# Optimization experiments

Hardware: AMD Instinct MI355X
Metric: run time of the kernel (lower is better)

Reference implementation:

```python
import jax, jax.numpy as jnp
import numpy as np

B, S, D = 8, 1024, 1024
H, Dh = 16, 64
NEG = 1e12


def setup_inputs() -> dict:
    key = jax.random.key(0)
    ks = jax.random.split(key, 8)
    scale = 0.02
    return {
        "Q": jax.random.normal(ks[0], (B, S, D), dtype=jnp.float32),
        "K": jax.random.normal(ks[1], (B, S, D), dtype=jnp.float32),
        "V": jax.random.normal(ks[2], (B, S, D), dtype=jnp.float32),
        "WQ": jax.random.normal(ks[3], (D, H * Dh), dtype=jnp.float32) * scale,
        "WK": jax.random.normal(ks[4], (D, H * Dh), dtype=jnp.float32) * scale,
        "WV": jax.random.normal(ks[5], (D, H * Dh), dtype=jnp.float32) * scale,
        "Q_len": jax.random.randint(ks[6], (B, 1), 0, S, dtype=jnp.int32),
        "V_len": jax.random.randint(ks[7], (B, 1), 0, S, dtype=jnp.int32),
    }


def reference(Q, K, V, WQ, WK, WV, Q_len, V_len):
    b, sq, _ = Q.shape
    sk = K.shape[1]
    # QKV projections -> [B, H, S, Dh]
    q = (Q @ WQ).reshape(b, sq, H, Dh).transpose(0, 2, 1, 3)
    k = (K @ WK).reshape(b, sk, H, Dh).transpose(0, 2, 1, 3)
    v = (V @ WV).reshape(b, sk, H, Dh).transpose(0, 2, 1, 3)
    # scaled scores [B, H, Sq, Sk]
    A = jnp.einsum("bhqd,bhkd->bhqk", q, k) / jnp.sqrt(jnp.float32(Dh))
    # key padding mask: valid where position < V_len (one_hot + cumsum equivalent)
    key_valid = (jnp.arange(sk)[None, :] < V_len[:, 0:1]).astype(A.dtype)  # [B, Sk]
    A = A - (1.0 - key_valid)[:, None, None, :] * NEG
    # causal mask (mask_right=True): mask strictly upper triangle
    causal = (jnp.arange(sq)[:, None] < jnp.arange(sk)[None, :]).astype(A.dtype)
    A = A - causal[None, None, :, :] * NEG
    A = jax.nn.softmax(A, axis=-1)
    O = jnp.einsum("bhqk,bhkd->bhqd", A, v)
    O = O.transpose(0, 2, 1, 3).reshape(b, sq, H * Dh)
    # query mask (multiplicative)
    q_valid = (jnp.arange(sq)[None, :] < Q_len[:, 0:1]).astype(O.dtype)  # [B, Sq]
    return O * q_valid[:, :, None]
```

## Files before the change

### kernel.cpp

```cpp
#include <hip/hip_runtime.h>
#include <hip/hip_bf16.h>


#define B_  8
#define S_  1024
#define D_  1024
#define H_  16
#define DH_ 64

using f16x8  = __attribute__((ext_vector_type(8))) _Float16;
using h16x2  = __attribute__((ext_vector_type(2))) __fp16;
using s16x8  = __attribute__((ext_vector_type(8))) short;
using f32x4  = __attribute__((ext_vector_type(4))) float;
using s16x4  = __attribute__((ext_vector_type(4))) short;

__device__ inline short f2h(float x) {
  _Float16 h = (_Float16)x;
  return __builtin_bit_cast(short, h);
}

__device__ inline unsigned pk2(float a, float b) {
  h16x2 p = __builtin_amdgcn_cvt_pkrtz(a, b);
  return __builtin_bit_cast(unsigned, p);
}

__device__ inline f16x8 ld_frag_g(const short* p) {
  return __builtin_bit_cast(f16x8, *(const s16x8*)p);
}

__device__ inline int kvlim_of(int vl, int ql) {
  const int v = (vl == 0) ? S_ : vl;
  return (v < ql) ? v : ql;
}

#define GLOAD_LDS16(gsrc, ldst)                                              \
  __builtin_amdgcn_global_load_lds(                                          \
      (const __attribute__((address_space(1))) unsigned int*)(gsrc),         \
      (__attribute__((address_space(3))) unsigned int*)(ldst), 16, 0, 0)

__global__ __launch_bounds__(256) void prep(
    const float* __restrict__ Qx, const float* __restrict__ Kx,
    const float* __restrict__ Vx, const float* __restrict__ WQ,
    const float* __restrict__ WK, const float* __restrict__ WV,
    short* __restrict__ dq, short* __restrict__ dk, short* __restrict__ dv,
    short* __restrict__ wt, short* __restrict__ qp, int* __restrict__ alist,
    const int* __restrict__ Qlen, const int* __restrict__ Vlen) {
  __shared__ float t[64][65];
  __shared__ int scnt[257];
  const int bid = blockIdx.x;
  const int tid = threadIdx.x;
  if (bid == 3840) {
    int ql[8], kv[8];
#pragma unroll
    for (int b = 0; b < 8; ++b) {
      ql[b] = Qlen[b];
      kv[b] = kvlim_of(Vlen[b], ql[b]);
    }
    int loc[6];
    int cnt = 0;
#pragma unroll
    for (int k = 0; k < 6; ++k) {
      const int c = tid * 6 + k;
      const int slice = c % 3, r = c / 3;
      bool act;
      if (slice < 2) {
        const int jm = r & 63;
        const int m0 = (jm & 7) * 1024 + (jm >> 3) * 128;
        const int len = slice ? kv[m0 >> 10] : ql[m0 >> 10];
        act = (m0 & 1023) < len;
      } else {
        const int jn = r >> 3;
        const int n0 = (jn & 7) * 1024 + (jn >> 3) * 128;
        act = (n0 & 1023) < kv[n0 >> 10];
      }
      if (act) loc[cnt++] = c;
    }
    scnt[tid] = cnt;
    __syncthreads();
    if (tid == 0) {
      int s = 0;
      for (int i = 0; i < 256; ++i) {
        const int v = scnt[i];
        scnt[i] = s;
        s += v;
      }
      scnt[256] = s;
    }
    __syncthreads();
    const int base = scnt[tid];
    for (int k = 0; k < cnt; ++k) alist[base + k] = loc[k];
    if (tid == 0) alist[1536] = scnt[256];
  } else if (bid < 3072) {
    const int slice = bid >> 10;
    const int tok0 = (bid & 1023) * 8;
    const int bb = tok0 >> 10, local = tok0 & 1023;
    const int ql = Qlen[bb];
    int lim;
    if (slice == 0) {
      lim = (ql + 127) & ~127;
    } else {
      lim = (kvlim_of(Vlen[bb], ql) + 127) & ~127;
    }
    if (local >= lim) {
      if (slice == 0) {
        const uint4 zz = {0u, 0u, 0u, 0u};
        const int hh = tid >> 4;
        short* zp = qp + ((size_t)((bb * H_ + hh) * S_) + local) * DH_ +
                    (tid & 15) * 32;
        *(uint4*)(zp + 0) = zz;
        *(uint4*)(zp + 8) = zz;
        *(uint4*)(zp + 16) = zz;
        *(uint4*)(zp + 24) = zz;
      }
      return;
    }
    const float* src = (slice == 0) ? Qx : (slice == 1) ? Kx : Vx;
    short* dst = (slice == 0) ? dq : (slice == 1) ? dk : dv;
    const size_t base = (size_t)(bid & 1023) * 8192;
#pragma unroll
    for (int j = 0; j < 4; ++j) {
      const size_t off = base + (size_t)j * 2048 + (size_t)tid * 8;
      float4 a = *(const float4*)(src + off);
      float4 b = *(const float4*)(src + off + 4);
      uint4 u = {pk2(a.x, a.y), pk2(a.z, a.w), pk2(b.x, b.y), pk2(b.z, b.w)};
      *(uint4*)(dst + off) = u;
    }
  } else {
    const int wid = bid - 3072;
    const int slice = wid >> 8;
    const int rem = wid & 255;
    const int n0 = (rem & 15) * 64, k0 = (rem >> 4) * 64;
    const float* W = (slice == 0) ? WQ : (slice == 1) ? WK : WV;
    {
      const int r = tid >> 2, c4 = tid & 3;
#pragma unroll
      for (int j = 0; j < 4; ++j) {
        float4 v = *(const float4*)(W + (size_t)(k0 + r) * D_ + n0 + c4 * 16 +
                                    j * 4);
        t[r][c4 * 16 + j * 4 + 0] = v.x;
        t[r][c4 * 16 + j * 4 + 1] = v.y;
        t[r][c4 * 16 + j * 4 + 2] = v.z;
        t[r][c4 * 16 + j * 4 + 3] = v.w;
      }
    }
    __syncthreads();
    {
      const int rn = tid >> 2, ks = tid & 3;
      short* dst =
          wt + ((size_t)slice << 20) + (size_t)(n0 + rn) * D_ + k0 + ks * 16;
      s16x4 h[4];
#pragma unroll
      for (int g = 0; g < 4; ++g)
#pragma unroll
        for (int j = 0; j < 4; ++j) h[g][j] = f2h(t[ks * 16 + g * 4 + j][rn]);
      *(s16x4*)(dst + 0) = h[0];
      *(s16x4*)(dst + 4) = h[1];
      *(s16x4*)(dst + 8) = h[2];
      *(s16x4*)(dst + 12) = h[3];
    }
  }
}

__global__ __launch_bounds__(256, 3) void proj(
    const short* __restrict__ xq, const short* __restrict__ xk,
    const short* __restrict__ xv, const short* __restrict__ wt,
    short* __restrict__ qp, short* __restrict__ kp, short* __restrict__ vp,
    const int* __restrict__ alist) {
  __shared__ __align__(16) short As[3][128][32];
  __shared__ __align__(16) short Bs[3][128][32];
  const int gid = blockIdx.x;
  if (gid >= alist[1536]) return;
  const int c = alist[gid];
  const int slice = c % 3;
  const int r = c / 3;
  const int tid = threadIdx.x;
  const short* A;
  const short* Bp;
  int m0, n0;
  float oscale;
  if (slice < 2) {
    A = slice ? xk : xq;
    Bp = wt + ((size_t)slice << 20);
    const int jm = r & 63;
    m0 = (jm & 7) * 1024 + (jm >> 3) * 128;
    n0 = (r >> 6) * 128;
    oscale = slice ? 1.0f : 0.125f;
  } else {
    A = wt + ((size_t)2 << 20);
    Bp = xv;
    m0 = (r & 7) * 128;
    const int jn = r >> 3;
    n0 = (jn & 7) * 1024 + (jn >> 3) * 128;
    oscale = 1.0f;
  }

  const int lane = tid & 63, w = tid >> 6;
  const int wr = w >> 1, wc = w & 1;
  const int lr = lane & 15, lg = lane >> 4;
  const int g_row = tid >> 2, g_c = tid & 3;
  const int gsw = (g_c ^ ((g_row >> 1) & 3)) * 8;
  const int rsw = (lg ^ ((lr >> 1) & 3)) * 8;

  const short* ga = A + (size_t)(m0 + g_row) * D_ + gsw;
  const short* gb = Bp + (size_t)(n0 + g_row) * D_ + gsw;

  f32x4 acc[4][4];
#pragma unroll
  for (int i = 0; i < 4; ++i)
#pragma unroll
    for (int j = 0; j < 4; ++j) acc[i][j] = f32x4{0.f, 0.f, 0.f, 0.f};

  GLOAD_LDS16(ga, &As[0][g_row][g_c * 8]);
  GLOAD_LDS16(ga + (size_t)64 * D_, &As[0][g_row + 64][g_c * 8]);
  GLOAD_LDS16(gb, &Bs[0][g_row][g_c * 8]);
  GLOAD_LDS16(gb + (size_t)64 * D_, &Bs[0][g_row + 64][g_c * 8]);
  GLOAD_LDS16(ga + 32, &As[1][g_row][g_c * 8]);
  GLOAD_LDS16(ga + (size_t)64 * D_ + 32, &As[1][g_row + 64][g_c * 8]);
  GLOAD_LDS16(gb + 32, &Bs[1][g_row][g_c * 8]);
  GLOAD_LDS16(gb + (size_t)64 * D_ + 32, &Bs[1][g_row + 64][g_c * 8]);

  for (int kt = 0; kt < 32; ++kt) {
    const int cur = kt % 3;
    if (kt < 30)
      asm volatile("s_waitcnt vmcnt(4)" ::: "memory");
    else
      asm volatile("s_waitcnt vmcnt(0)" ::: "memory");
    __builtin_amdgcn_s_barrier();
    __builtin_amdgcn_sched_barrier(0);
    if (kt < 30) {
      const int pre = (kt + 2) % 3;
      const int k2 = (kt + 2) * 32;
      GLOAD_LDS16(ga + k2, &As[pre][g_row][g_c * 8]);
      GLOAD_LDS16(ga + (size_t)64 * D_ + k2, &As[pre][g_row + 64][g_c * 8]);
      GLOAD_LDS16(gb + k2, &Bs[pre][g_row][g_c * 8]);
      GLOAD_LDS16(gb + (size_t)64 * D_ + k2, &Bs[pre][g_row + 64][g_c * 8]);
    }

    f16x8 af[4], bf[4];
#pragma unroll
    for (int mi = 0; mi < 4; ++mi)
      af[mi] = ld_frag_g(&As[cur][wr * 64 + mi * 16 + lr][rsw]);
#pragma unroll
    for (int ni = 0; ni < 4; ++ni)
      bf[ni] = ld_frag_g(&Bs[cur][wc * 64 + ni * 16 + lr][rsw]);
#pragma unroll
    for (int mi = 0; mi < 4; ++mi)
#pragma unroll
      for (int ni = 0; ni < 4; ++ni)
        acc[mi][ni] = __builtin_amdgcn_mfma_f32_16x16x32_f16(
            af[mi], bf[ni], acc[mi][ni], 0, 0, 0);
  }

  short* outp = (slice == 0) ? qp : kp;
#pragma unroll
  for (int mi = 0; mi < 4; ++mi)
#pragma unroll
    for (int ni = 0; ni < 4; ++ni) {
      const int mg0 = m0 + wr * 64 + mi * 16 + lg * 4;
      const int ng = n0 + wc * 64 + ni * 16 + lr;
#pragma unroll
      for (int reg = 0; reg < 4; ++reg) {
        const int m = mg0 + reg;
        const short val = f2h(acc[mi][ni][reg] * oscale);
        if (slice < 2) {
          const int b = m >> 10, s = m & 1023, hh = ng >> 6, dh = ng & 63;
          outp[((size_t)((b * H_ + hh) * S_) + s) * DH_ + dh] = val;
        } else {
          vp[((size_t)(ng >> 10) << 20) + (size_t)m * S_ + (ng & 1023)] = val;
        }
      }
    }
}

__global__ __launch_bounds__(256, 2) void attn_fwd(
    const short* __restrict__ qp, const short* __restrict__ kp,
    const short* __restrict__ vT, const int* __restrict__ Qlen,
    const int* __restrict__ Vlen, float* __restrict__ out) {
  __shared__ short Plds[2][4][16][72];
  const int bid = blockIdx.x;
  const int z = bid & 7;
  const int bh = bid >> 3;
  const int h = bh & 15;
  const int b = bh >> 4;
  const int lane = threadIdx.x & 63;
  const int w = threadIdx.x >> 6;
  const int lr = lane & 15, lg = lane >> 4;
  const short* qb = qp + (size_t)((b * H_ + h) * S_) * DH_;
  const short* kb = kp + (size_t)((b * H_ + h) * S_) * DH_;
  const short* vb = vT + (size_t)((b * H_ + h) * DH_) * S_;
  const int vlen = Vlen[b], qlen = Qlen[b];

  const int qtH = 15 - z, qtL = z;
  const int vcap = (vlen + 63) >> 6;
  const int nTH = (vlen > 0) ? min(qtH + 1, vcap) : (qtH + 1);
  const int nTL = (vlen > 0) ? min(qtL + 1, vcap) : (qtL + 1);
  const int q0H = qtH * 64 + w * 16;
  const int q0L = qtL * 64 + w * 16;

  const bool hAct = qlen > qtH * 64;
  const bool lAct = qlen > qtL * 64;
  const int tHn = hAct ? nTH : 0;
  const int tLn = lAct ? nTL : 0;
  const int tMax = (tHn > tLn) ? tHn : tLn;

  f16x8 qfH[2], qfL[2];
#pragma unroll
  for (int c = 0; c < 2; ++c) {
    qfH[c] = ld_frag_g(qb + (size_t)(q0H + lr) * DH_ + c * 32 + lg * 8);
    qfL[c] = ld_frag_g(qb + (size_t)(q0L + lr) * DH_ + c * 32 + lg * 8);
  }

  float lH[4], lL[4];
  f32x4 oH[4], oL[4];
#pragma unroll
  for (int rr = 0; rr < 4; ++rr) {
    lH[rr] = 0.f; lL[rr] = 0.f;
    oH[rr] = f32x4{0.f, 0.f, 0.f, 0.f};
    oL[rr] = f32x4{0.f, 0.f, 0.f, 0.f};
  }

  f16x8 kf[8];
#pragma unroll
  for (int nt = 0; nt < 4; ++nt)
#pragma unroll
    for (int c = 0; c < 2; ++c)
      kf[nt * 2 + c] =
          ld_frag_g(kb + (size_t)(nt * 16 + lr) * DH_ + c * 32 + lg * 8);

  for (int t = 0; t < tMax; ++t) {
    const int kv0 = t * 64;
    const int kvn = (t + 1 < tMax) ? kv0 + 64 : kv0;
    const bool hact = t < tHn;
    const bool lact = t < tLn;

    f16x8 vf[8];
#pragma unroll
    for (int dt = 0; dt < 4; ++dt)
#pragma unroll
      for (int c = 0; c < 2; ++c)
        vf[dt * 2 + c] =
            ld_frag_g(vb + (size_t)(dt * 16 + lr) * S_ + kv0 + c * 32 + lg * 8);

    f16x8 kn[8];
#pragma unroll
    for (int nt = 0; nt < 4; ++nt)
#pragma unroll
      for (int c = 0; c < 2; ++c)
        kn[nt * 2 + c] = ld_frag_g(kb + (size_t)(kvn + nt * 16 + lr) * DH_ +
                                   c * 32 + lg * 8);

    const bool km = (vlen > 0) && (vlen - kv0 < 64);

    f32x4 sH[4], sL[4];
    if (hact) {
#pragma unroll
      for (int nt = 0; nt < 4; ++nt) sH[nt] = f32x4{0.f, 0.f, 0.f, 0.f};
#pragma unroll
      for (int nt = 0; nt < 4; ++nt)
#pragma unroll
        for (int c = 0; c < 2; ++c)
          sH[nt] = __builtin_amdgcn_mfma_f32_16x16x32_f16(
              qfH[c], kf[nt * 2 + c], sH[nt], 0, 0, 0);
    }
    if (lact) {
#pragma unroll
      for (int nt = 0; nt < 4; ++nt) sL[nt] = f32x4{0.f, 0.f, 0.f, 0.f};
#pragma unroll
      for (int nt = 0; nt < 4; ++nt)
#pragma unroll
        for (int c = 0; c < 2; ++c)
          sL[nt] = __builtin_amdgcn_mfma_f32_16x16x32_f16(
              qfL[c], kf[nt * 2 + c], sL[nt], 0, 0, 0);
    }

    if (hact) {
      if ((t == qtH) | km) {
#pragma unroll
        for (int reg = 0; reg < 4; ++reg) {
          const int qrow = q0H + lg * 4 + reg;
#pragma unroll
          for (int nt = 0; nt < 4; ++nt) {
            const int kv = kv0 + nt * 16 + lr;
            float sv = sH[nt][reg];
            if (km && kv >= vlen) sv -= 1e12f;
            if (kv > qrow) sv -= 1e12f;
            const float p = __expf(sv);
            lH[reg] += p;
            Plds[0][w][lg * 4 + reg][nt * 16 + lr] = f2h(p);
          }
        }
      } else {
#pragma unroll
        for (int reg = 0; reg < 4; ++reg)
#pragma unroll
          for (int nt = 0; nt < 4; ++nt) {
            const float p = __expf(sH[nt][reg]);
            lH[reg] += p;
            Plds[0][w][lg * 4 + reg][nt * 16 + lr] = f2h(p);
          }
      }
    }
    if (lact) {
      if ((t == qtL) | km) {
#pragma unroll
        for (int reg = 0; reg < 4; ++reg) {
          const int qrow = q0L + lg * 4 + reg;
#pragma unroll
          for (int nt = 0; nt < 4; ++nt) {
            const int kv = kv0 + nt * 16 + lr;
            float sv = sL[nt][reg];
            if (km && kv >= vlen) sv -= 1e12f;
            if (kv > qrow) sv -= 1e12f;
            const float p = __expf(sv);
            lL[reg] += p;
            Plds[1][w][lg * 4 + reg][nt * 16 + lr] = f2h(p);
          }
        }
      } else {
#pragma unroll
        for (int reg = 0; reg < 4; ++reg)
#pragma unroll
          for (int nt = 0; nt < 4; ++nt) {
            const float p = __expf(sL[nt][reg]);
            lL[reg] += p;
            Plds[1][w][lg * 4 + reg][nt * 16 + lr] = f2h(p);
          }
      }
    }

    if (hact) {
#pragma unroll
      for (int c = 0; c < 2; ++c) {
        s16x4 a0 = *(const s16x4*)(&Plds[0][w][lr][c * 32 + lg * 8]);
        s16x4 a1 = *(const s16x4*)(&Plds[0][w][lr][c * 32 + lg * 8 + 4]);
        s16x8 pr = {a0[0], a0[1], a0[2], a0[3], a1[0], a1[1], a1[2], a1[3]};
        f16x8 paH = __builtin_bit_cast(f16x8, pr);
#pragma unroll
        for (int dt = 0; dt < 4; ++dt)
          oH[dt] = __builtin_amdgcn_mfma_f32_16x16x32_f16(paH, vf[dt * 2 + c],
                                                          oH[dt], 0, 0, 0);
      }
    }
    if (lact) {
#pragma unroll
      for (int c = 0; c < 2; ++c) {
        s16x4 a0 = *(const s16x4*)(&Plds[1][w][lr][c * 32 + lg * 8]);
        s16x4 a1 = *(const s16x4*)(&Plds[1][w][lr][c * 32 + lg * 8 + 4]);
        s16x8 pr = {a0[0], a0[1], a0[2], a0[3], a1[0], a1[1], a1[2], a1[3]};
        f16x8 paL = __builtin_bit_cast(f16x8, pr);
#pragma unroll
        for (int dt = 0; dt < 4; ++dt)
          oL[dt] = __builtin_amdgcn_mfma_f32_16x16x32_f16(paL, vf[dt * 2 + c],
                                                          oL[dt], 0, 0, 0);
      }
    }

#pragma unroll
    for (int i = 0; i < 8; ++i) kf[i] = kn[i];
  }

#pragma unroll
  for (int reg = 0; reg < 4; ++reg) {
    float ls = lH[reg];
    ls += __shfl_xor(ls, 1);
    ls += __shfl_xor(ls, 2);
    ls += __shfl_xor(ls, 4);
    ls += __shfl_xor(ls, 8);
    const int qrow = q0H + lg * 4 + reg;
    const float sc = (qrow < qlen) ? (1.f / ls) : 0.f;
#pragma unroll
    for (int dt = 0; dt < 4; ++dt)
      out[(size_t)(b * S_ + qrow) * D_ + h * DH_ + dt * 16 + lr] =
          oH[dt][reg] * sc;
  }
#pragma unroll
  for (int reg = 0; reg < 4; ++reg) {
    float ls = lL[reg];
    ls += __shfl_xor(ls, 1);
    ls += __shfl_xor(ls, 2);
    ls += __shfl_xor(ls, 4);
    ls += __shfl_xor(ls, 8);
    const int qrow = q0L + lg * 4 + reg;
    const float sc = (qrow < qlen) ? (1.f / ls) : 0.f;
#pragma unroll
    for (int dt = 0; dt < 4; ++dt)
      out[(size_t)(b * S_ + qrow) * D_ + h * DH_ + dt * 16 + lr] =
          oL[dt][reg] * sc;
  }
}

extern "C" void kernel_launch(void* const* d_in, const int* in_sizes, int n_in,
                              void* d_out, int out_size, void* d_ws,
                              size_t ws_size, hipStream_t stream) {
  const float* Q = (const float*)d_in[0];
  const float* K = (const float*)d_in[1];
  const float* V = (const float*)d_in[2];
  const float* WQ = (const float*)d_in[3];
  const float* WK = (const float*)d_in[4];
  const float* WV = (const float*)d_in[5];
  const int* Qlen = (const int*)d_in[6];
  const int* Vlen = (const int*)d_in[7];
  float* out = (float*)d_out;

  const size_t PE = (size_t)B_ * H_ * S_ * DH_;
  short* qp = (short*)d_ws;
  short* kp = qp + PE;
  short* vT = kp + PE;
  short* wt = vT + PE;
  short* xhV = wt + 3 * 1048576;
  int* alist = (int*)(xhV + PE);
  short* xhQ = (short*)d_out;
  short* xhK = xhQ + PE;

  prep<<<dim3(3841), dim3(256), 0, stream>>>(Q, K, V, WQ, WK, WV, xhQ, xhK,
                                             xhV, wt, qp, alist, Qlen, Vlen);
  proj<<<dim3(1536), dim3(256), 0, stream>>>(xhQ, xhK, xhV, wt, qp, kp, vT,
                                             alist);
  attn_fwd<<<dim3(1024), dim3(256), 0, stream>>>(qp, kp, vT, Qlen, Vlen, out);
}
```

Before: 103.1 us.

## Schedule attention blocks from compacted active-tile list, zero inactive rows directly

The prep kernel now builds a compacted list of (batch, query-tile) pairs that have valid query rows, plus a list of inactive ones. Attention blocks each handle one query tile per head, ordered longest first, instead of pairing a high and a low tile per block. Inactive tiles launch lightweight blocks that write zeros to the output, so the prep kernel no longer zeroes projected-Q padding. Occupancy is raised to three blocks per CU. The cost is an extra indirection read at kernel start and a larger launch grid, some of whose blocks exit immediately.

```diff
diff --git a/kernel.cpp b/kernel.cpp
--- a/kernel.cpp
+++ b/kernel.cpp
@@ -43,8 +43,9 @@
     const float* __restrict__ Vx, const float* __restrict__ WQ,
     const float* __restrict__ WK, const float* __restrict__ WV,
     short* __restrict__ dq, short* __restrict__ dk, short* __restrict__ dv,
-    short* __restrict__ wt, short* __restrict__ qp, int* __restrict__ alist,
-    const int* __restrict__ Qlen, const int* __restrict__ Vlen) {
+    short* __restrict__ wt, int* __restrict__ alist, int* __restrict__ alist2,
+    int* __restrict__ zlist, const int* __restrict__ Qlen,
+    const int* __restrict__ Vlen) {
   __shared__ float t[64][65];
   __shared__ int scnt[257];
   const int bid = blockIdx.x;
@@ -89,7 +90,19 @@
     __syncthreads();
     const int base = scnt[tid];
     for (int k = 0; k < cnt; ++k) alist[base + k] = loc[k];
-    if (tid == 0) alist[1536] = scnt[256];
+    if (tid == 0) {
+      alist[1536] = scnt[256];
+      int c2 = 0, zc = 0;
+      for (int k = 0; k < 128; ++k) {
+        const int qt = 15 - (k >> 3), b = k & 7;
+        if (qt * 64 < ql[b])
+          alist2[c2++] = (b << 4) | qt;
+        else
+          zlist[zc++] = (b << 4) | qt;
+      }
+      alist2[128] = c2;
+      zlist[128] = zc;
+    }
   } else if (bid < 3072) {
     const int slice = bid >> 10;
     const int tok0 = (bid & 1023) * 8;
@@ -101,19 +114,7 @@
     } else {
       lim = (kvlim_of(Vlen[bb], ql) + 127) & ~127;
     }
-    if (local >= lim) {
-      if (slice == 0) {
-        const uint4 zz = {0u, 0u, 0u, 0u};
-        const int hh = tid >> 4;
-        short* zp = qp + ((size_t)((bb * H_ + hh) * S_) + local) * DH_ +
-                    (tid & 15) * 32;
-        *(uint4*)(zp + 0) = zz;
-        *(uint4*)(zp + 8) = zz;
-        *(uint4*)(zp + 16) = zz;
-        *(uint4*)(zp + 24) = zz;
-      }
-      return;
-    }
+    if (local >= lim) return;
     const float* src = (slice == 0) ? Qx : (slice == 1) ? Kx : Vx;
     short* dst = (slice == 0) ? dq : (slice == 1) ? dk : dv;
     const size_t base = (size_t)(bid & 1023) * 8192;
@@ -272,51 +273,53 @@
     }
 }
 
-__global__ __launch_bounds__(256, 2) void attn_fwd(
+__global__ __launch_bounds__(256, 3) void attn_fwd(
     const short* __restrict__ qp, const short* __restrict__ kp,
     const short* __restrict__ vT, const int* __restrict__ Qlen,
-    const int* __restrict__ Vlen, float* __restrict__ out) {
-  __shared__ short Plds[2][4][16][72];
-  const int bid = blockIdx.x;
-  const int z = bid & 7;
-  const int bh = bid >> 3;
-  const int h = bh & 15;
-  const int b = bh >> 4;
-  const int lane = threadIdx.x & 63;
-  const int w = threadIdx.x >> 6;
+    const int* __restrict__ Vlen, float* __restrict__ out,
+    const int* __restrict__ alist2, const int* __restrict__ zlist) {
+  __shared__ short Plds[4][16][72];
+  const int g = blockIdx.x;
+  const int cnt2 = alist2[128];
+  const int tid = threadIdx.x;
+  if (g >= 16 * cnt2) {
+    const int zg = g - 16 * cnt2;
+    if (zg >= 4 * zlist[128]) return;
+    const int e = zlist[zg >> 2];
+    const int b = e >> 4, qt = e & 15;
+    const int row0 = qt * 64 + (zg & 3) * 16;
+    float* ob = out + (size_t)(b * S_ + row0) * D_;
+    const float4 zf = {0.f, 0.f, 0.f, 0.f};
+#pragma unroll
+    for (int i = 0; i < 16; ++i)
+      *(float4*)(ob + (size_t)(i * 256 + tid) * 4) = zf;
+    return;
+  }
+  const int e = alist2[g >> 4];
+  const int h = g & 15;
+  const int b = e >> 4, qt = e & 15;
+  const int lane = tid & 63;
+  const int w = tid >> 6;
   const int lr = lane & 15, lg = lane >> 4;
   const short* qb = qp + (size_t)((b * H_ + h) * S_) * DH_;
   const short* kb = kp + (size_t)((b * H_ + h) * S_) * DH_;
   const short* vb = vT + (size_t)((b * H_ + h) * DH_) * S_;
   const int vlen = Vlen[b], qlen = Qlen[b];
-
-  const int qtH = 15 - z, qtL = z;
   const int vcap = (vlen + 63) >> 6;
-  const int nTH = (vlen > 0) ? min(qtH + 1, vcap) : (qtH + 1);
-  const int nTL = (vlen > 0) ? min(qtL + 1, vcap) : (qtL + 1);
-  const int q0H = qtH * 64 + w * 16;
-  const int q0L = qtL * 64 + w * 16;
-
-  const bool hAct = qlen > qtH * 64;
-  const bool lAct = qlen > qtL * 64;
-  const int tHn = hAct ? nTH : 0;
-  const int tLn = lAct ? nTL : 0;
-  const int tMax = (tHn > tLn) ? tHn : tLn;
-
-  f16x8 qfH[2], qfL[2];
-#pragma unroll
-  for (int c = 0; c < 2; ++c) {
-    qfH[c] = ld_frag_g(qb + (size_t)(q0H + lr) * DH_ + c * 32 + lg * 8);
-    qfL[c] = ld_frag_g(qb + (size_t)(q0L + lr) * DH_ + c * 32 + lg * 8);
-  }
-
-  float lH[4], lL[4];
-  f32x4 oH[4], oL[4];
+  const int nT = (vlen > 0) ? min(qt + 1, vcap) : (qt + 1);
+  const int q0 = qt * 64 + w * 16;
+
+  f16x8 qf[2];
+#pragma unroll
+  for (int c = 0; c < 2; ++c)
+    qf[c] = ld_frag_g(qb + (size_t)(q0 + lr) * DH_ + c * 32 + lg * 8);
+
+  float l[4];
+  f32x4 o[4];
 #pragma unroll
   for (int rr = 0; rr < 4; ++rr) {
-    lH[rr] = 0.f; lL[rr] = 0.f;
-    oH[rr] = f32x4{0.f, 0.f, 0.f, 0.f};
-    oL[rr] = f32x4{0.f, 0.f, 0.f, 0.f};
+    l[rr] = 0.f;
+    o[rr] = f32x4{0.f, 0.f, 0.f, 0.f};
   }
 
   f16x8 kf[8];
@@ -327,11 +330,9 @@
       kf[nt * 2 + c] =
           ld_frag_g(kb + (size_t)(nt * 16 + lr) * DH_ + c * 32 + lg * 8);
 
-  for (int t = 0; t < tMax; ++t) {
+  for (int t = 0; t < nT; ++t) {
     const int kv0 = t * 64;
-    const int kvn = (t + 1 < tMax) ? kv0 + 64 : kv0;
-    const bool hact = t < tHn;
-    const bool lact = t < tLn;
+    const int kvn = (t + 1 < nT) ? kv0 + 64 : kv0;
 
     f16x8 vf[8];
 #pragma unroll
@@ -349,110 +350,53 @@
         kn[nt * 2 + c] = ld_frag_g(kb + (size_t)(kvn + nt * 16 + lr) * DH_ +
                                    c * 32 + lg * 8);
 
+    f32x4 s[4];
+#pragma unroll
+    for (int nt = 0; nt < 4; ++nt) s[nt] = f32x4{0.f, 0.f, 0.f, 0.f};
+#pragma unroll
+    for (int nt = 0; nt < 4; ++nt)
+#pragma unroll
+      for (int c = 0; c < 2; ++c)
+        s[nt] = __builtin_amdgcn_mfma_f32_16x16x32_f16(qf[c], kf[nt * 2 + c],
+                                                       s[nt], 0, 0, 0);
+
     const bool km = (vlen > 0) && (vlen - kv0 < 64);
-
-    f32x4 sH[4], sL[4];
-    if (hact) {
-#pragma unroll
-      for (int nt = 0; nt < 4; ++nt) sH[nt] = f32x4{0.f, 0.f, 0.f, 0.f};
-#pragma unroll
-      for (int nt = 0; nt < 4; ++nt)
-#pragma unroll
-        for (int c = 0; c < 2; ++c)
-          sH[nt] = __builtin_amdgcn_mfma_f32_16x16x32_f16(
-              qfH[c], kf[nt * 2 + c], sH[nt], 0, 0, 0);
-    }
-    if (lact) {
-#pragma unroll
-      for (int nt = 0; nt < 4; ++nt) sL[nt] = f32x4{0.f, 0.f, 0.f, 0.f};
-#pragma unroll
-      for (int nt = 0; nt < 4; ++nt)
-#pragma unroll
-        for (int c = 0; c < 2; ++c)
-          sL[nt] = __builtin_amdgcn_mfma_f32_16x16x32_f16(
-              qfL[c], kf[nt * 2 + c], sL[nt], 0, 0, 0);
-    }
-
-    if (hact) {
-      if ((t == qtH) | km) {
-#pragma unroll
-        for (int reg = 0; reg < 4; ++reg) {
-          const int qrow = q0H + lg * 4 + reg;
-#pragma unroll
-          for (int nt = 0; nt < 4; ++nt) {
-            const int kv = kv0 + nt * 16 + lr;
-            float sv = sH[nt][reg];
-            if (km && kv >= vlen) sv -= 1e12f;
-            if (kv > qrow) sv -= 1e12f;
-            const float p = __expf(sv);
-            lH[reg] += p;
-            Plds[0][w][lg * 4 + reg][nt * 16 + lr] = f2h(p);
-          }
+    if ((t == qt) | km) {
+#pragma unroll
+      for (int reg = 0; reg < 4; ++reg) {
+        const int qrow = q0 + lg * 4 + reg;
+#pragma unroll
+        for (int nt = 0; nt < 4; ++nt) {
+          const int kv = kv0 + nt * 16 + lr;
+          float sv = s[nt][reg];
+          if (km && kv >= vlen) sv -= 1e12f;
+          if (kv > qrow) sv -= 1e12f;
+          const float p = __expf(sv);
+          l[reg] += p;
+          Plds[w][lg * 4 + reg][nt * 16 + lr] = f2h(p);
         }
-      } else {
-#pragma unroll
-        for (int reg = 0; reg < 4; ++reg)
-#pragma unroll
-          for (int nt = 0; nt < 4; ++nt) {
-            const float p = __expf(sH[nt][reg]);
-            lH[reg] += p;
-            Plds[0][w][lg * 4 + reg][nt * 16 + lr] = f2h(p);
-          }
-      }
-    }
-    if (lact) {
-      if ((t == qtL) | km) {
-#pragma unroll
-        for (int reg = 0; reg < 4; ++reg) {
-          const int qrow = q0L + lg * 4 + reg;
-#pragma unroll
-          for (int nt = 0; nt < 4; ++nt) {
-            const int kv = kv0 + nt * 16 + lr;
-            float sv = sL[nt][reg];
-            if (km && kv >= vlen) sv -= 1e12f;
-            if (kv > qrow) sv -= 1e12f;
-            const float p = __expf(sv);
-            lL[reg] += p;
-            Plds[1][w][lg * 4 + reg][nt * 16 + lr] = f2h(p);
-          }
+      }
+    } else {
+#pragma unroll
+      for (int reg = 0; reg < 4; ++reg)
+#pragma unroll
+        for (int nt = 0; nt < 4; ++nt) {
+          const float p = __expf(s[nt][reg]);
+          l[reg] += p;
+          Plds[w][lg * 4 + reg][nt * 16 + lr] = f2h(p);
         }
-      } else {
-#pragma unroll
-        for (int reg = 0; reg < 4; ++reg)
-#pragma unroll
-          for (int nt = 0; nt < 4; ++nt) {
-            const float p = __expf(sL[nt][reg]);
-            lL[reg] += p;
-            Plds[1][w][lg * 4 + reg][nt * 16 + lr] = f2h(p);
-          }
-      }
-    }
-
-    if (hact) {
-#pragma unroll
-      for (int c = 0; c < 2; ++c) {
-        s16x4 a0 = *(const s16x4*)(&Plds[0][w][lr][c * 32 + lg * 8]);
-        s16x4 a1 = *(const s16x4*)(&Plds[0][w][lr][c * 32 + lg * 8 + 4]);
-        s16x8 pr = {a0[0], a0[1], a0[2], a0[3], a1[0], a1[1], a1[2], a1[3]};
-        f16x8 paH = __builtin_bit_cast(f16x8, pr);
-#pragma unroll
-        for (int dt = 0; dt < 4; ++dt)
-          oH[dt] = __builtin_amdgcn_mfma_f32_16x16x32_f16(paH, vf[dt * 2 + c],
-                                                          oH[dt], 0, 0, 0);
-      }
-    }
-    if (lact) {
-#pragma unroll
-      for (int c = 0; c < 2; ++c) {
-        s16x4 a0 = *(const s16x4*)(&Plds[1][w][lr][c * 32 + lg * 8]);
-        s16x4 a1 = *(const s16x4*)(&Plds[1][w][lr][c * 32 + lg * 8 + 4]);
-        s16x8 pr = {a0[0], a0[1], a0[2], a0[3], a1[0], a1[1], a1[2], a1[3]};
-        f16x8 paL = __builtin_bit_cast(f16x8, pr);
-#pragma unroll
-        for (int dt = 0; dt < 4; ++dt)
-          oL[dt] = __builtin_amdgcn_mfma_f32_16x16x32_f16(paL, vf[dt * 2 + c],
-                                                          oL[dt], 0, 0, 0);
-      }
+    }
+
+#pragma unroll
+    for (int c = 0; c < 2; ++c) {
+      s16x4 a0 = *(const s16x4*)(&Plds[w][lr][c * 32 + lg * 8]);
+      s16x4 a1 = *(const s16x4*)(&Plds[w][lr][c * 32 + lg * 8 + 4]);
+      s16x8 pr = {a0[0], a0[1], a0[2], a0[3], a1[0], a1[1], a1[2], a1[3]};
+      f16x8 pa = __builtin_bit_cast(f16x8, pr);
+#pragma unroll
+      for (int dt = 0; dt < 4; ++dt)
+        o[dt] = __builtin_amdgcn_mfma_f32_16x16x32_f16(pa, vf[dt * 2 + c],
+                                                       o[dt], 0, 0, 0);
     }
 
 #pragma unroll
@@ -461,31 +405,17 @@
 
 #pragma unroll
   for (int reg = 0; reg < 4; ++reg) {
-    float ls = lH[reg];
+    float ls = l[reg];
     ls += __shfl_xor(ls, 1);
     ls += __shfl_xor(ls, 2);
     ls += __shfl_xor(ls, 4);
     ls += __shfl_xor(ls, 8);
-    const int qrow = q0H + lg * 4 + reg;
+    const int qrow = q0 + lg * 4 + reg;
     const float sc = (qrow < qlen) ? (1.f / ls) : 0.f;
 #pragma unroll
     for (int dt = 0; dt < 4; ++dt)
       out[(size_t)(b * S_ + qrow) * D_ + h * DH_ + dt * 16 + lr] =
-          oH[dt][reg] * sc;
-  }
-#pragma unroll
-  for (int reg = 0; reg < 4; ++reg) {
-    float ls = lL[reg];
-    ls += __shfl_xor(ls, 1);
-    ls += __shfl_xor(ls, 2);
-    ls += __shfl_xor(ls, 4);
-    ls += __shfl_xor(ls, 8);
-    const int qrow = q0L + lg * 4 + reg;
-    const float sc = (qrow < qlen) ? (1.f / ls) : 0.f;
-#pragma unroll
-    for (int dt = 0; dt < 4; ++dt)
-      out[(size_t)(b * S_ + qrow) * D_ + h * DH_ + dt * 16 + lr] =
-          oL[dt][reg] * sc;
+          o[dt][reg] * sc;
   }
 }
 
@@ -509,12 +439,16 @@
   short* wt = vT + PE;
   short* xhV = wt + 3 * 1048576;
   int* alist = (int*)(xhV + PE);
+  int* alist2 = alist + 1540;
+  int* zlist = alist2 + 132;
   short* xhQ = (short*)d_out;
   short* xhK = xhQ + PE;
 
   prep<<<dim3(3841), dim3(256), 0, stream>>>(Q, K, V, WQ, WK, WV, xhQ, xhK,
-                                             xhV, wt, qp, alist, Qlen, Vlen);
+                                             xhV, wt, alist, alist2, zlist,
+                                             Qlen, Vlen);
   proj<<<dim3(1536), dim3(256), 0, stream>>>(xhQ, xhK, xhV, wt, qp, kp, vT,
                                              alist);
-  attn_fwd<<<dim3(1024), dim3(256), 0, stream>>>(qp, kp, vT, Qlen, Vlen, out);
-}
+  attn_fwd<<<dim3(2560), dim3(256), 0, stream>>>(qp, kp, vT, Qlen, Vlen, out,
+                                                 alist2, zlist);
+}
```

Result: slower. 119.2 us (+15.6%).

## Stage K/V tiles into swizzled LDS with triple-buffered async global-to-LDS loads

Applied to the files above, without the earlier changes.

Replaces per-wave direct global fragment loads of K and V, where each wave redundantly fetched the same tiles, with a cooperative block-wide staging of each 64x64 K and V tile into LDS. Staging uses direct global-to-LDS loads with a triple buffer two tiles ahead and XOR-swizzled columns to avoid bank conflicts. The P scratch buffer is shrunk to one shared slot reused for the high and low query tiles. This aims to cut redundant global/L2 traffic and hide load latency. In exchange it adds a block barrier per iteration and much more LDS use, about 50KB, which may limit occupancy to fewer than 2 blocks per CU.

```diff
diff --git a/kernel.cpp b/kernel.cpp
--- a/kernel.cpp
+++ b/kernel.cpp
@@ -276,14 +276,17 @@
     const short* __restrict__ qp, const short* __restrict__ kp,
     const short* __restrict__ vT, const int* __restrict__ Qlen,
     const int* __restrict__ Vlen, float* __restrict__ out) {
-  __shared__ short Plds[2][4][16][72];
+  __shared__ __align__(16) short Ks[3][64][64];
+  __shared__ __align__(16) short Vs[3][64][64];
+  __shared__ short Plds[4][16][72];
   const int bid = blockIdx.x;
   const int z = bid & 7;
   const int bh = bid >> 3;
   const int h = bh & 15;
   const int b = bh >> 4;
-  const int lane = threadIdx.x & 63;
-  const int w = threadIdx.x >> 6;
+  const int tid = threadIdx.x;
+  const int lane = tid & 63;
+  const int w = tid >> 6;
   const int lr = lane & 15, lg = lane >> 4;
   const short* qb = qp + (size_t)((b * H_ + h) * S_) * DH_;
   const short* kb = kp + (size_t)((b * H_ + h) * S_) * DH_;
@@ -303,6 +306,23 @@
   const int tLn = lAct ? nTL : 0;
   const int tMax = (tHn > tLn) ? tHn : tLn;
 
+  const int s_r0 = w * 16 + (lane >> 3);
+  const int s_g = lane & 7;
+
+#define STAGEKV(buf, s)                                                       \
+  do {                                                                        \
+    const int kv0s = (s) * 64;                                                \
+    const int r0_ = s_r0, r1_ = s_r0 + 8;                                     \
+    const int sg0_ = (s_g ^ (r0_ & 7)) * 8;                                   \
+    const int sg1_ = (s_g ^ (r1_ & 7)) * 8;                                   \
+    GLOAD_LDS16(kb + (size_t)(kv0s + r0_) * DH_ + sg0_,                       \
+                &Ks[buf][r0_][s_g * 8]);                                      \
+    GLOAD_LDS16(vb + (size_t)r0_ * S_ + kv0s + sg0_, &Vs[buf][r0_][s_g * 8]); \
+    GLOAD_LDS16(kb + (size_t)(kv0s + r1_) * DH_ + sg1_,                       \
+                &Ks[buf][r1_][s_g * 8]);                                      \
+    GLOAD_LDS16(vb + (size_t)r1_ * S_ + kv0s + sg1_, &Vs[buf][r1_][s_g * 8]); \
+  } while (0)
+
   f16x8 qfH[2], qfL[2];
 #pragma unroll
   for (int c = 0; c < 2; ++c) {
@@ -319,145 +339,142 @@
     oL[rr] = f32x4{0.f, 0.f, 0.f, 0.f};
   }
 
-  f16x8 kf[8];
-#pragma unroll
-  for (int nt = 0; nt < 4; ++nt)
-#pragma unroll
-    for (int c = 0; c < 2; ++c)
-      kf[nt * 2 + c] =
-          ld_frag_g(kb + (size_t)(nt * 16 + lr) * DH_ + c * 32 + lg * 8);
-
-  for (int t = 0; t < tMax; ++t) {
-    const int kv0 = t * 64;
-    const int kvn = (t + 1 < tMax) ? kv0 + 64 : kv0;
-    const bool hact = t < tHn;
-    const bool lact = t < tLn;
-
-    f16x8 vf[8];
-#pragma unroll
-    for (int dt = 0; dt < 4; ++dt)
-#pragma unroll
-      for (int c = 0; c < 2; ++c)
-        vf[dt * 2 + c] =
-            ld_frag_g(vb + (size_t)(dt * 16 + lr) * S_ + kv0 + c * 32 + lg * 8);
-
-    f16x8 kn[8];
-#pragma unroll
-    for (int nt = 0; nt < 4; ++nt)
-#pragma unroll
-      for (int c = 0; c < 2; ++c)
-        kn[nt * 2 + c] = ld_frag_g(kb + (size_t)(kvn + nt * 16 + lr) * DH_ +
-                                   c * 32 + lg * 8);
-
-    const bool km = (vlen > 0) && (vlen - kv0 < 64);
-
-    f32x4 sH[4], sL[4];
-    if (hact) {
-#pragma unroll
-      for (int nt = 0; nt < 4; ++nt) sH[nt] = f32x4{0.f, 0.f, 0.f, 0.f};
+  if (tMax > 0) {
+    STAGEKV(0, 0);
+    STAGEKV(1, (1 < tMax) ? 1 : 0);
+
+    for (int t = 0; t < tMax; ++t) {
+      const int cur = t % 3;
+      if (t < tMax - 2)
+        asm volatile("s_waitcnt vmcnt(4)" ::: "memory");
+      else
+        asm volatile("s_waitcnt vmcnt(0)" ::: "memory");
+      __builtin_amdgcn_s_barrier();
+      __builtin_amdgcn_sched_barrier(0);
+      if (t < tMax - 2) {
+        STAGEKV((t + 2) % 3, t + 2);
+      }
+
+      const int kv0 = t * 64;
+      const bool hact = t < tHn;
+      const bool lact = t < tLn;
+      const bool km = (vlen > 0) && (vlen - kv0 < 64);
+
+      f16x8 kf[8], vf[8];
 #pragma unroll
       for (int nt = 0; nt < 4; ++nt)
 #pragma unroll
         for (int c = 0; c < 2; ++c)
-          sH[nt] = __builtin_amdgcn_mfma_f32_16x16x32_f16(
-              qfH[c], kf[nt * 2 + c], sH[nt], 0, 0, 0);
-    }
-    if (lact) {
-#pragma unroll
-      for (int nt = 0; nt < 4; ++nt) sL[nt] = f32x4{0.f, 0.f, 0.f, 0.f};
-#pragma unroll
-      for (int nt = 0; nt < 4; ++nt)
+          kf[nt * 2 + c] = ld_frag_g(
+              &Ks[cur][nt * 16 + lr][((c * 4 + lg) ^ (lr & 7)) * 8]);
+#pragma unroll
+      for (int dt = 0; dt < 4; ++dt)
 #pragma unroll
         for (int c = 0; c < 2; ++c)
-          sL[nt] = __builtin_amdgcn_mfma_f32_16x16x32_f16(
-              qfL[c], kf[nt * 2 + c], sL[nt], 0, 0, 0);
-    }
-
-    if (hact) {
-      if ((t == qtH) | km) {
-#pragma unroll
-        for (int reg = 0; reg < 4; ++reg) {
-          const int qrow = q0H + lg * 4 + reg;
-#pragma unroll
-          for (int nt = 0; nt < 4; ++nt) {
-            const int kv = kv0 + nt * 16 + lr;
-            float sv = sH[nt][reg];
-            if (km && kv >= vlen) sv -= 1e12f;
-            if (kv > qrow) sv -= 1e12f;
-            const float p = __expf(sv);
-            lH[reg] += p;
-            Plds[0][w][lg * 4 + reg][nt * 16 + lr] = f2h(p);
+          vf[dt * 2 + c] = ld_frag_g(
+              &Vs[cur][dt * 16 + lr][((c * 4 + lg) ^ (lr & 7)) * 8]);
+
+      f32x4 sH[4], sL[4];
+      if (hact) {
+#pragma unroll
+        for (int nt = 0; nt < 4; ++nt) sH[nt] = f32x4{0.f, 0.f, 0.f, 0.f};
+#pragma unroll
+        for (int nt = 0; nt < 4; ++nt)
+#pragma unroll
+          for (int c = 0; c < 2; ++c)
+            sH[nt] = __builtin_amdgcn_mfma_f32_16x16x32_f16(
+                qfH[c], kf[nt * 2 + c], sH[nt], 0, 0, 0);
+      }
+      if (lact) {
+#pragma unroll
+        for (int nt = 0; nt < 4; ++nt) sL[nt] = f32x4{0.f, 0.f, 0.f, 0.f};
+#pragma unroll
+        for (int nt = 0; nt < 4; ++nt)
+#pragma unroll
+          for (int c = 0; c < 2; ++c)
+            sL[nt] = __builtin_amdgcn_mfma_f32_16x16x32_f16(
+                qfL[c], kf[nt * 2 + c], sL[nt], 0, 0, 0);
+      }
+
+      if (hact) {
+        if ((t == qtH) | km) {
+#pragma unroll
+          for (int reg = 0; reg < 4; ++reg) {
+            const int qrow = q0H + lg * 4 + reg;
+#pragma unroll
+            for (int nt = 0; nt < 4; ++nt) {
+              const int kv = kv0 + nt * 16 + lr;
+              float sv = sH[nt][reg];
+              if (km && kv >= vlen) sv -= 1e12f;
+              if (kv > qrow) sv -= 1e12f;
+              const float p = __expf(sv);
+              lH[reg] += p;
+              Plds[w][lg * 4 + reg][nt * 16 + lr] = f2h(p);
+            }
           }
+        } else {
+#pragma unroll
+          for (int reg = 0; reg < 4; ++reg)
+#pragma unroll
+            for (int nt = 0; nt < 4; ++nt) {
+              const float p = __expf(sH[nt][reg]);
+              lH[reg] += p;
+              Plds[w][lg * 4 + reg][nt * 16 + lr] = f2h(p);
+            }
         }
-      } else {
-#pragma unroll
-        for (int reg = 0; reg < 4; ++reg)
-#pragma unroll
-          for (int nt = 0; nt < 4; ++nt) {
-            const float p = __expf(sH[nt][reg]);
-            lH[reg] += p;
-            Plds[0][w][lg * 4 + reg][nt * 16 + lr] = f2h(p);
+#pragma unroll
+        for (int c = 0; c < 2; ++c) {
+          s16x4 a0 = *(const s16x4*)(&Plds[w][lr][c * 32 + lg * 8]);
+          s16x4 a1 = *(const s16x4*)(&Plds[w][lr][c * 32 + lg * 8 + 4]);
+          s16x8 pr = {a0[0], a0[1], a0[2], a0[3], a1[0], a1[1], a1[2], a1[3]};
+          f16x8 pa = __builtin_bit_cast(f16x8, pr);
+#pragma unroll
+          for (int dt = 0; dt < 4; ++dt)
+            oH[dt] = __builtin_amdgcn_mfma_f32_16x16x32_f16(pa, vf[dt * 2 + c],
+                                                            oH[dt], 0, 0, 0);
+        }
+      }
+      if (lact) {
+        if ((t == qtL) | km) {
+#pragma unroll
+          for (int reg = 0; reg < 4; ++reg) {
+            const int qrow = q0L + lg * 4 + reg;
+#pragma unroll
+            for (int nt = 0; nt < 4; ++nt) {
+              const int kv = kv0 + nt * 16 + lr;
+              float sv = sL[nt][reg];
+              if (km && kv >= vlen) sv -= 1e12f;
+              if (kv > qrow) sv -= 1e12f;
+              const float p = __expf(sv);
+              lL[reg] += p;
+              Plds[w][lg * 4 + reg][nt * 16 + lr] = f2h(p);
+            }
           }
-      }
-    }
-    if (lact) {
-      if ((t == qtL) | km) {
-#pragma unroll
-        for (int reg = 0; reg < 4; ++reg) {
-          const int qrow = q0L + lg * 4 + reg;
-#pragma unroll
-          for (int nt = 0; nt < 4; ++nt) {
-            const int kv = kv0 + nt * 16 + lr;
-            float sv = sL[nt][reg];
-            if (km && kv >= vlen) sv -= 1e12f;
-            if (kv > qrow) sv -= 1e12f;
-            const float p = __expf(sv);
-            lL[reg] += p;
-            Plds[1][w][lg * 4 + reg][nt * 16 + lr] = f2h(p);
-          }
+        } else {
+#pragma unroll
+          for (int reg = 0; reg < 4; ++reg)
+#pragma unroll
+            for (int nt = 0; nt < 4; ++nt) {
+              const float p = __expf(sL[nt][reg]);
+              lL[reg] += p;
+              Plds[w][lg * 4 + reg][nt * 16 + lr] = f2h(p);
+            }
         }
-      } else {
-#pragma unroll
-        for (int reg = 0; reg < 4; ++reg)
-#pragma unroll
-          for (int nt = 0; nt < 4; ++nt) {
-            const float p = __expf(sL[nt][reg]);
-            lL[reg] += p;
-            Plds[1][w][lg * 4 + reg][nt * 16 + lr] = f2h(p);
-          }
-      }
-    }
-
-    if (hact) {
-#pragma unroll
-      for (int c = 0; c < 2; ++c) {
-        s16x4 a0 = *(const s16x4*)(&Plds[0][w][lr][c * 32 + lg * 8]);
-        s16x4 a1 = *(const s16x4*)(&Plds[0][w][lr][c * 32 + lg * 8 + 4]);
-        s16x8 pr = {a0[0], a0[1], a0[2], a0[3], a1[0], a1[1], a1[2], a1[3]};
-        f16x8 paH = __builtin_bit_cast(f16x8, pr);
-#pragma unroll
-        for (int dt = 0; dt < 4; ++dt)
-          oH[dt] = __builtin_amdgcn_mfma_f32_16x16x32_f16(paH, vf[dt * 2 + c],
-                                                          oH[dt], 0, 0, 0);
-      }
-    }
-    if (lact) {
-#pragma unroll
-      for (int c = 0; c < 2; ++c) {
-        s16x4 a0 = *(const s16x4*)(&Plds[1][w][lr][c * 32 + lg * 8]);
-        s16x4 a1 = *(const s16x4*)(&Plds[1][w][lr][c * 32 + lg * 8 + 4]);
-        s16x8 pr = {a0[0], a0[1], a0[2], a0[3], a1[0], a1[1], a1[2], a1[3]};
-        f16x8 paL = __builtin_bit_cast(f16x8, pr);
-#pragma unroll
-        for (int dt = 0; dt < 4; ++dt)
-          oL[dt] = __builtin_amdgcn_mfma_f32_16x16x32_f16(paL, vf[dt * 2 + c],
-                                                          oL[dt], 0, 0, 0);
-      }
-    }
-
-#pragma unroll
-    for (int i = 0; i < 8; ++i) kf[i] = kn[i];
-  }
+#pragma unroll
+        for (int c = 0; c < 2; ++c) {
+          s16x4 a0 = *(const s16x4*)(&Plds[w][lr][c * 32 + lg * 8]);
+          s16x4 a1 = *(const s16x4*)(&Plds[w][lr][c * 32 + lg * 8 + 4]);
+          s16x8 pr = {a0[0], a0[1], a0[2], a0[3], a1[0], a1[1], a1[2], a1[3]};
+          f16x8 pa = __builtin_bit_cast(f16x8, pr);
+#pragma unroll
+          for (int dt = 0; dt < 4; ++dt)
+            oL[dt] = __builtin_amdgcn_mfma_f32_16x16x32_f16(pa, vf[dt * 2 + c],
+                                                            oL[dt], 0, 0, 0);
+        }
+      }
+    }
+  }
+#undef STAGEKV
 
 #pragma unroll
   for (int reg = 0; reg < 4; ++reg) {
```

After: 85.47 us (median of 2 runs). 17.1% less time.
